# Kernel tuning notes

Measured on AMD Instinct MI355X. Metric: run time of the kernel, lower is better.

Reference implementation:

```python
import jax, jax.numpy as jnp
import numpy as np


def setup_inputs() -> dict:
    key = jax.random.key(0)
    k1, k2, k3 = jax.random.split(key, 3)
    n, c, h, w = 32, 384, 56, 56
    m, d_model = 8, 768
    x = jax.random.normal(k1, (n, c, h, w), dtype=jnp.float32)
    global_feature = jax.random.normal(k2, (n, m, d_model), dtype=jnp.float32)
    # Linear(d_model, 2*c): torch weight shape (2c, d_model)
    W_kv = jax.random.normal(k3, (2 * c, d_model), dtype=jnp.float32) * (1.0 / np.sqrt(d_model))
    b_kv = jnp.zeros((2 * c,), dtype=jnp.float32)
    return {"x": x, "global_feature": global_feature, "W_kv": W_kv, "b_kv": b_kv}


def reference(x, global_feature, W_kv, b_kv):
    n, c, h, w = x.shape
    # MLP (single Linear + ReLU6, no BN since bn=False)
    kv = jnp.einsum('nmd,ed->nme', global_feature, W_kv) + b_kv  # [n, m, 2c]
    kv = jnp.clip(kv, 0.0, 6.0)  # ReLU6
    K = kv[:, :, :c]   # [n, m, c]
    V = kv[:, :, c:]   # [n, m, c]
    q = x.reshape(n, c, h * w).transpose(0, 2, 1)  # [n, hw, c]
    scores = jnp.einsum('nqc,nkc->nqk', q, K)       # [n, hw, m] (unscaled)
    attn = jax.nn.softmax(scores, axis=-1)
    v_agg = jnp.einsum('nqk,nkc->nqc', attn, V)     # [n, hw, c]
    feature = v_agg.transpose(0, 2, 1).reshape(n, c, h, w)
    return feature + x
```

## Files before the change

kernel.cpp:

```cpp
#include <hip/hip_runtime.h>


#define NC 384
#define HWP 3136
#define DD 768
#define MM 8
#define EE 768

__global__ __launch_bounds__(256) void kv_kernel(const float* __restrict__ gf,
                                                 const float* __restrict__ Wk,
                                                 const float* __restrict__ bk,
                                                 float* __restrict__ kv) {
    __shared__ float g[MM * DD];
    const int n = blockIdx.y;
    const int et = blockIdx.x;
    const int t = threadIdx.x;

    const float* gfn = gf + (size_t)n * (MM * DD);
    for (int i = t; i < MM * DD; i += 256) g[i] = gfn[i];
    __syncthreads();

    const int e = et * 64 + (t & 63);
    const int mb = (t >> 6) * 2;

    const float4* w4 = (const float4*)(Wk + (size_t)e * DD);
    const float4* g0 = (const float4*)(g + (mb + 0) * DD);
    const float4* g1 = (const float4*)(g + (mb + 1) * DD);

    float a0 = 0.f, a1 = 0.f;
    #pragma unroll 8
    for (int i = 0; i < DD / 4; ++i) {
        const float4 w = w4[i];
        const float4 v0 = g0[i];
        const float4 v1 = g1[i];
        a0 += w.x * v0.x + w.y * v0.y + w.z * v0.z + w.w * v0.w;
        a1 += w.x * v1.x + w.y * v1.y + w.z * v1.z + w.w * v1.w;
    }
    const float bv = bk[e];
    float* o = kv + (size_t)n * (MM * EE);
    o[(mb + 0) * EE + e] = fminf(fmaxf(a0 + bv, 0.f), 6.f);
    o[(mb + 1) * EE + e] = fminf(fmaxf(a1 + bv, 0.f), 6.f);
}

__global__ __launch_bounds__(256, 6) void attn_kernel(const float* __restrict__ x,
                                                      const float* __restrict__ kv,
                                                      float* __restrict__ out) {
    __shared__ float kvs[6656];

    const int n = blockIdx.y;
    const int tile = blockIdx.x;
    const int t = threadIdx.x;
    const int lane = t & 63;
    const int w = t >> 6;
    const int g = lane >> 3;
    const int pos = tile * 32 + w * 8 + (lane & 7);
    const int c0 = g * 48;

    const float4* kvn4 = (const float4*)(kv + (size_t)n * (MM * EE));
    #pragma unroll
    for (int r = 0; r < 6; ++r) {
        const int f = t + r * 256;
        const int k = f / 192;
        const int e4 = f - k * 192;
        const int half = (e4 >= 96) ? 1 : 0;
        const int c4 = e4 - half * 96;
        const int g2 = c4 / 12;
        const int j4 = c4 - g2 * 12;
        *(float4*)&kvs[half * 3328 + k * 416 + g2 * 52 + j4 * 4] = kvn4[f];
    }
    __syncthreads();

    const float* xp = x + (size_t)n * NC * HWP + (size_t)c0 * HWP + pos;
    float xr[48];
    #pragma unroll
    for (int i = 0; i < 48; ++i) xr[i] = xp[(size_t)i * HWP];

    float acc[8];
    #pragma unroll
    for (int k = 0; k < 8; ++k) acc[k] = 0.f;

    const float* kbase = &kvs[g * 52];
    #pragma unroll
    for (int i4 = 0; i4 < 12; ++i4) {
        const float x0 = xr[i4 * 4 + 0];
        const float x1 = xr[i4 * 4 + 1];
        const float x2 = xr[i4 * 4 + 2];
        const float x3 = xr[i4 * 4 + 3];
        #pragma unroll
        for (int k = 0; k < 8; ++k) {
            const float4 kk = *(const float4*)&kbase[k * 416 + i4 * 4];
            acc[k] += x0 * kk.x + x1 * kk.y + x2 * kk.z + x3 * kk.w;
        }
    }

    #pragma unroll
    for (int k = 0; k < 8; ++k) {
        acc[k] += __shfl_xor(acc[k], 8, 64);
        acc[k] += __shfl_xor(acc[k], 16, 64);
        acc[k] += __shfl_xor(acc[k], 32, 64);
    }

    {
        float mx = acc[0];
        #pragma unroll
        for (int k = 1; k < 8; ++k) mx = fmaxf(mx, acc[k]);
        float su = 0.f;
        #pragma unroll
        for (int k = 0; k < 8; ++k) { acc[k] = __expf(acc[k] - mx); su += acc[k]; }
        const float inv = 1.f / su;
        #pragma unroll
        for (int k = 0; k < 8; ++k) acc[k] *= inv;
    }

    float* op = out + (size_t)n * NC * HWP + (size_t)c0 * HWP + pos;
    const float* vbase = &kvs[3328 + g * 52];
    #pragma unroll
    for (int i4 = 0; i4 < 12; ++i4) {
        float o0 = xr[i4 * 4 + 0];
        float o1 = xr[i4 * 4 + 1];
        float o2 = xr[i4 * 4 + 2];
        float o3 = xr[i4 * 4 + 3];
        #pragma unroll
        for (int k = 0; k < 8; ++k) {
            const float4 vv = *(const float4*)&vbase[k * 416 + i4 * 4];
            o0 += acc[k] * vv.x;
            o1 += acc[k] * vv.y;
            o2 += acc[k] * vv.z;
            o3 += acc[k] * vv.w;
        }
        op[(size_t)(i4 * 4 + 0) * HWP] = o0;
        op[(size_t)(i4 * 4 + 1) * HWP] = o1;
        op[(size_t)(i4 * 4 + 2) * HWP] = o2;
        op[(size_t)(i4 * 4 + 3) * HWP] = o3;
    }
}

extern "C" void kernel_launch(void* const* d_in, const int* in_sizes, int n_in,
                              void* d_out, int out_size, void* d_ws, size_t ws_size,
                              hipStream_t stream) {
    const float* x  = (const float*)d_in[0];
    const float* gf = (const float*)d_in[1];
    const float* Wk = (const float*)d_in[2];
    const float* bk = (const float*)d_in[3];
    float* out = (float*)d_out;
    float* kv = (float*)d_ws;

    kv_kernel<<<dim3(12, 32), 256, 0, stream>>>(gf, Wk, bk, kv);
    attn_kernel<<<dim3(98, 32), 256, 0, stream>>>(x, kv, out);
}
```

Baseline: 359.2 us.

## Process four spatial positions per thread with float4 loads, re-reading x for residual

Each thread now handles four consecutive spatial positions, using float4 global loads and stores in place of scalar strided accesses. Blocks shrink to 128 threads and the grid halves, so each K/V value read from shared memory is reused across four positions. The x register cache is dropped and x is read a second time from global memory (likely an L2 hit) for the residual, which lowers register pressure but adds memory traffic. Each block loads the same shared kv table for twice as many positions, and total parallelism falls.

```diff
diff --git a/kernel.cpp b/kernel.cpp
--- a/kernel.cpp
+++ b/kernel.cpp
@@ -42,7 +42,7 @@
     o[(mb + 1) * EE + e] = fminf(fmaxf(a1 + bv, 0.f), 6.f);
 }
 
-__global__ __launch_bounds__(256, 6) void attn_kernel(const float* __restrict__ x,
+__global__ __launch_bounds__(128, 3) void attn_kernel(const float* __restrict__ x,
                                                       const float* __restrict__ kv,
                                                       float* __restrict__ out) {
     __shared__ float kvs[6656];
@@ -53,13 +53,13 @@
     const int lane = t & 63;
     const int w = t >> 6;
     const int g = lane >> 3;
-    const int pos = tile * 32 + w * 8 + (lane & 7);
     const int c0 = g * 48;
+    const int pos0 = tile * 64 + w * 32 + (lane & 7) * 4;
 
     const float4* kvn4 = (const float4*)(kv + (size_t)n * (MM * EE));
     #pragma unroll
-    for (int r = 0; r < 6; ++r) {
-        const int f = t + r * 256;
+    for (int r = 0; r < 12; ++r) {
+        const int f = t + r * 128;
         const int k = f / 192;
         const int e4 = f - k * 192;
         const int half = (e4 >= 96) ? 1 : 0;
@@ -70,68 +70,77 @@
     }
     __syncthreads();
 
-    const float* xp = x + (size_t)n * NC * HWP + (size_t)c0 * HWP + pos;
-    float xr[48];
+    const float* xp = x + (size_t)n * NC * HWP + (size_t)c0 * HWP + pos0;
+    float acc[8][4];
     #pragma unroll
-    for (int i = 0; i < 48; ++i) xr[i] = xp[(size_t)i * HWP];
-
-    float acc[8];
-    #pragma unroll
-    for (int k = 0; k < 8; ++k) acc[k] = 0.f;
+    for (int k = 0; k < 8; ++k)
+        #pragma unroll
+        for (int p = 0; p < 4; ++p) acc[k][p] = 0.f;
 
     const float* kbase = &kvs[g * 52];
     #pragma unroll
     for (int i4 = 0; i4 < 12; ++i4) {
-        const float x0 = xr[i4 * 4 + 0];
-        const float x1 = xr[i4 * 4 + 1];
-        const float x2 = xr[i4 * 4 + 2];
-        const float x3 = xr[i4 * 4 + 3];
+        const float4 xa = *(const float4*)(xp + (size_t)(i4 * 4 + 0) * HWP);
+        const float4 xb = *(const float4*)(xp + (size_t)(i4 * 4 + 1) * HWP);
+        const float4 xc = *(const float4*)(xp + (size_t)(i4 * 4 + 2) * HWP);
+        const float4 xd = *(const float4*)(xp + (size_t)(i4 * 4 + 3) * HWP);
         #pragma unroll
         for (int k = 0; k < 8; ++k) {
             const float4 kk = *(const float4*)&kbase[k * 416 + i4 * 4];
-            acc[k] += x0 * kk.x + x1 * kk.y + x2 * kk.z + x3 * kk.w;
+            acc[k][0] += xa.x * kk.x + xb.x * kk.y + xc.x * kk.z + xd.x * kk.w;
+            acc[k][1] += xa.y * kk.x + xb.y * kk.y + xc.y * kk.z + xd.y * kk.w;
+            acc[k][2] += xa.z * kk.x + xb.z * kk.y + xc.z * kk.z + xd.z * kk.w;
+            acc[k][3] += xa.w * kk.x + xb.w * kk.y + xc.w * kk.z + xd.w * kk.w;
         }
     }
 
     #pragma unroll
     for (int k = 0; k < 8; ++k) {
-        acc[k] += __shfl_xor(acc[k], 8, 64);
-        acc[k] += __shfl_xor(acc[k], 16, 64);
-        acc[k] += __shfl_xor(acc[k], 32, 64);
+        #pragma unroll
+        for (int p = 0; p < 4; ++p) {
+            acc[k][p] += __shfl_xor(acc[k][p], 8, 64);
+            acc[k][p] += __shfl_xor(acc[k][p], 16, 64);
+            acc[k][p] += __shfl_xor(acc[k][p], 32, 64);
+        }
     }
 
-    {
-        float mx = acc[0];
+    #pragma unroll
+    for (int p = 0; p < 4; ++p) {
+        float mx = acc[0][p];
         #pragma unroll
-        for (int k = 1; k < 8; ++k) mx = fmaxf(mx, acc[k]);
+        for (int k = 1; k < 8; ++k) mx = fmaxf(mx, acc[k][p]);
         float su = 0.f;
         #pragma unroll
-        for (int k = 0; k < 8; ++k) { acc[k] = __expf(acc[k] - mx); su += acc[k]; }
+        for (int k = 0; k < 8; ++k) { acc[k][p] = __expf(acc[k][p] - mx); su += acc[k][p]; }
         const float inv = 1.f / su;
         #pragma unroll
-        for (int k = 0; k < 8; ++k) acc[k] *= inv;
+        for (int k = 0; k < 8; ++k) acc[k][p] *= inv;
     }
 
-    float* op = out + (size_t)n * NC * HWP + (size_t)c0 * HWP + pos;
+    float* op = out + (size_t)n * NC * HWP + (size_t)c0 * HWP + pos0;
     const float* vbase = &kvs[3328 + g * 52];
-    #pragma unroll
+    #pragma unroll 6
     for (int i4 = 0; i4 < 12; ++i4) {
-        float o0 = xr[i4 * 4 + 0];
-        float o1 = xr[i4 * 4 + 1];
-        float o2 = xr[i4 * 4 + 2];
-        float o3 = xr[i4 * 4 + 3];
+        float4 oa = *(const float4*)(xp + (size_t)(i4 * 4 + 0) * HWP);
+        float4 ob = *(const float4*)(xp + (size_t)(i4 * 4 + 1) * HWP);
+        float4 oc = *(const float4*)(xp + (size_t)(i4 * 4 + 2) * HWP);
+        float4 od = *(const float4*)(xp + (size_t)(i4 * 4 + 3) * HWP);
         #pragma unroll
         for (int k = 0; k < 8; ++k) {
             const float4 vv = *(const float4*)&vbase[k * 416 + i4 * 4];
-            o0 += acc[k] * vv.x;
-            o1 += acc[k] * vv.y;
-            o2 += acc[k] * vv.z;
-            o3 += acc[k] * vv.w;
+            oa.x += acc[k][0] * vv.x; oa.y += acc[k][1] * vv.x;
+            oa.z += acc[k][2] * vv.x; oa.w += acc[k][3] * vv.x;
+            ob.x += acc[k][0] * vv.y; ob.y += acc[k][1] * vv.y;
+            ob.z += acc[k][2] * vv.y; ob.w += acc[k][3] * vv.y;
+            oc.x += acc[k][0] * vv.z; oc.y += acc[k][1] * vv.z;
+            oc.z += acc[k][2] * vv.z; oc.w += acc[k][3] * vv.z;
+            od.x += acc[k][0] * vv.w; od.y += acc[k][1] * vv.w;
+            od.z += acc[k][2] * vv.w; od.w += acc[k][3] * vv.w;
         }
-        op[(size_t)(i4 * 4 + 0) * HWP] = o0;
-        op[(size_t)(i4 * 4 + 1) * HWP] = o1;
-        op[(size_t)(i4 * 4 + 2) * HWP] = o2;
-        op[(size_t)(i4 * 4 + 3) * HWP] = o3;
+        *(float4*)(op + (size_t)(i4 * 4 + 0) * HWP) = oa;
+        *(float4*)(op + (size_t)(i4 * 4 + 1) * HWP) = ob;
+        *(float4*)(op + (size_t)(i4 * 4 + 2) * HWP) = oc;
+        *(float4*)(op + (size_t)(i4 * 4 + 3) * HWP) = od;
     }
 }
 
@@ -146,5 +155,5 @@
     float* kv = (float*)d_ws;
 
     kv_kernel<<<dim3(12, 32), 256, 0, stream>>>(gf, Wk, bk, kv);
-    attn_kernel<<<dim3(98, 32), 256, 0, stream>>>(x, kv, out);
+    attn_kernel<<<dim3(49, 32), 128, 0, stream>>>(x, kv, out);
 }
```

New measurement: 513.3 us. 1.43x slower.
